# Optimization experiments

Measured on AMD Instinct MI355X. Metric: run time of the kernel, lower is better.

## Reference

```python
import jax, jax.numpy as jnp
import numpy as np


def setup_inputs() -> dict:
    key = jax.random.key(0)
    ks = jax.random.split(key, 7)
    B, IN, OUT, G = 8192, 2048, 2048, 4
    s_i = 1.0 / np.sqrt(IN)
    s_h = 1.0 / np.sqrt(OUT)
    return {
        "x": jax.random.normal(ks[0], (B, IN), jnp.float32),
        "prev_h": jax.random.normal(ks[1], (B, OUT), jnp.float32),
        "prev_c": jax.random.normal(ks[2], (B, OUT), jnp.float32),
        "Wi": jax.random.normal(ks[3], (G, IN, OUT), jnp.float32) * s_i,
        "Wh": jax.random.normal(ks[4], (G, OUT, OUT), jnp.float32) * s_h,
        "bi": jax.random.normal(ks[5], (G, OUT), jnp.float32) * s_i,
        "bh": jax.random.normal(ks[6], (G, OUT), jnp.float32) * s_h,
    }


def reference(x, prev_h, prev_c, Wi, Wh, bi, bh):
    # Two fused GEMMs replacing 8 per-gate Linears (gate order: in, forget, in2, out)
    # gates: [B, 4, OUT]
    gates = (jnp.einsum("bi,gio->bgo", x, Wi) + bi[None]
             + jnp.einsum("bh,gho->bgo", prev_h, Wh) + bh[None])
    in_gate = jax.nn.sigmoid(gates[:, 0])
    forget_gate = jax.nn.sigmoid(gates[:, 1])
    in_gate2 = jax.nn.sigmoid(gates[:, 2])
    out_gate = jax.nn.sigmoid(gates[:, 3])
    next_c = forget_gate * prev_c + in_gate * in_gate2
    # NOTE: faithful to source: out_gate + tanh(next_c) (addition, not multiply)
    next_h = out_gate + jnp.tanh(next_c)
    return next_h, next_c
```

## Files before the change

### kernel.cpp

```cpp
#include <hip/hip_runtime.h>
#include <stdint.h>


#define SZ_ELEMS 16777216
#define HALF_OUT 16777216

typedef __attribute__((ext_vector_type(8))) short bf16x8;
typedef __attribute__((ext_vector_type(4))) float f32x4;
typedef __attribute__((ext_vector_type(8))) unsigned short u16x8;

__device__ __forceinline__ unsigned short f2bf(float f) {
  unsigned int u = __float_as_uint(f);
  u += 0x7FFFu + ((u >> 16) & 1u);
  return (unsigned short)(u >> 16);
}

__device__ __forceinline__ void async16(const void* g, void* l) {
  __builtin_amdgcn_global_load_lds(
      (const __attribute__((address_space(1))) void*)g,
      (__attribute__((address_space(3))) void*)l, 16, 0, 0);
}

__device__ __forceinline__ float sigm(float x) { return 1.f / (1.f + __expf(-x)); }

__global__ void cvt_bf16_kernel(const float* __restrict__ src,
                                unsigned short* __restrict__ dst, int n4) {
  int i = blockIdx.x * blockDim.x + threadIdx.x;
  int stride = gridDim.x * blockDim.x;
  for (; i < n4; i += stride) {
    float4 v = reinterpret_cast<const float4*>(src)[i];
    ushort4 o;
    o.x = f2bf(v.x); o.y = f2bf(v.y); o.z = f2bf(v.z); o.w = f2bf(v.w);
    reinterpret_cast<ushort4*>(dst)[i] = o;
  }
}

__global__ void transpose_w_kernel(const float* __restrict__ Wi, const float* __restrict__ Wh,
                                   unsigned short* __restrict__ Wit, unsigned short* __restrict__ Wht) {
  __shared__ float tile[64][65];
  const int tk = blockIdx.x, to = blockIdx.y, gz = blockIdx.z;
  const float* W = (gz < 4 ? Wi : Wh) + (size_t)(gz & 3) * 4194304;
  unsigned short* Wt = (gz < 4 ? Wit : Wht) + (size_t)(gz & 3) * 4194304;
  const int t = threadIdx.x;
  const int o = t & 63, kr = t >> 6;
#pragma unroll
  for (int p = 0; p < 16; ++p) {
    int k = p * 4 + kr;
    tile[k][o] = W[(size_t)(tk * 64 + k) * 2048 + to * 64 + o];
  }
  __syncthreads();
#pragma unroll
  for (int p = 0; p < 2; ++p) {
    int idx = p * 256 + t;
    int orow = idx >> 3, k0 = (idx & 7) * 8;
    u16x8 v;
#pragma unroll
    for (int i = 0; i < 8; ++i) v[i] = f2bf(tile[k0 + i][orow]);
    *reinterpret_cast<u16x8*>(&Wt[(size_t)(to * 64 + orow) * 2048 + tk * 64 + k0]) = v;
  }
}

#define FENCE asm volatile("" ::: "memory")
#define BARRIER do { FENCE; __builtin_amdgcn_s_barrier(); FENCE; } while (0)
#define VMC6  asm volatile("s_waitcnt vmcnt(6)" ::: "memory")
#define VMC0  asm volatile("s_waitcnt vmcnt(0)" ::: "memory")

__global__ __launch_bounds__(512, 2) void lstm_gemm_kernel(
    const unsigned short* __restrict__ xb, const unsigned short* __restrict__ hb,
    const unsigned short* __restrict__ wit, const unsigned short* __restrict__ wht,
    const float* __restrict__ bi, const float* __restrict__ bh,
    const float* __restrict__ prev_c, float* __restrict__ out) {
  __shared__ char lds[131072];

  const int tid = threadIdx.x;
  const int wave = tid >> 6, lane = tid & 63;
  const int wm = wave >> 2, wn = wave & 3;
  const int bm = blockIdx.x;
  const int bo = blockIdx.y;

  const int kwin = (lane >> 4) << 4;
  const int fswz = (lane & 7) << 4;
  int aro[8], bro[4];
#pragma unroll
  for (int mf = 0; mf < 8; ++mf) aro[mf] = (wm * 128 + mf * 16 + (lane & 15)) * 128;
#pragma unroll
  for (int nf = 0; nf < 4; ++nf) bro[nf] = 32768 + (nf * 64 + wn * 16 + (lane & 15)) * 128;

  const int L0 = tid * 16;
  int agoff[2][2], bgoff[2][2];
#pragma unroll
  for (int h = 0; h < 2; ++h)
#pragma unroll
    for (int j = 0; j < 2; ++j) {
      int L = j * 8192 + L0;
      int row = h * 128 + (L >> 7);
      int c = (L & 127) ^ ((row & 7) << 4);
      agoff[h][j] = row * 4096 + c;
      int g = row >> 6, orow = row & 63;
      bgoff[h][j] = g * 8388608 + orow * 4096 + c;
    }
  const char* pxa = (const char*)xb + (size_t)bm * 1048576;
  const char* pha = (const char*)hb + (size_t)bm * 1048576;
  const char* pwi = (const char*)wit + (size_t)bo * 262144;
  const char* pwh = (const char*)wht + (size_t)bo * 262144;

  auto stageA = [&](int t, int h, int buf) {
    const char* base = (t < 32) ? (pxa + t * 128) : (pha + (t - 32) * 128);
    char* d = lds + buf * 65536 + h * 16384 + L0;
    async16(base + agoff[h][0], d);
    async16(base + agoff[h][1], d + 8192);
  };
  auto stageB = [&](int t, int h, int buf) {
    const char* base = (t < 32) ? (pwi + t * 128) : (pwh + (t - 32) * 128);
    char* d = lds + buf * 65536 + 32768 + h * 16384 + L0;
    async16(base + bgoff[h][0], d);
    async16(base + bgoff[h][1], d + 8192);
  };

  f32x4 acc[8][4];
  const f32x4 zero = {0.f, 0.f, 0.f, 0.f};
#pragma unroll
  for (int mf = 0; mf < 8; ++mf)
#pragma unroll
    for (int nf = 0; nf < 4; ++nf) acc[mf][nf] = zero;

  bf16x8 afrA[4][2];
  bf16x8 afrB[4][2];
  bf16x8 bfr[4][2];

  auto loadAA = [&](int buf) {
    const char* l = lds + buf * 65536;
#pragma unroll
    for (int m = 0; m < 4; ++m)
#pragma unroll
      for (int ks = 0; ks < 2; ++ks)
        afrA[m][ks] = *(const bf16x8*)(l + aro[m] + ((ks * 64 + kwin) ^ fswz));
  };
  auto loadAB = [&](int buf) {
    const char* l = lds + buf * 65536;
#pragma unroll
    for (int m = 0; m < 4; ++m)
#pragma unroll
      for (int ks = 0; ks < 2; ++ks)
        afrB[m][ks] = *(const bf16x8*)(l + aro[4 + m] + ((ks * 64 + kwin) ^ fswz));
  };
  auto loadB0 = [&](int buf) {
    const char* l = lds + buf * 65536;
#pragma unroll
    for (int n = 0; n < 2; ++n)
#pragma unroll
      for (int ks = 0; ks < 2; ++ks)
        bfr[n][ks] = *(const bf16x8*)(l + bro[n] + ((ks * 64 + kwin) ^ fswz));
  };
  auto loadB1 = [&](int buf) {
    const char* l = lds + buf * 65536;
#pragma unroll
    for (int n = 0; n < 2; ++n)
#pragma unroll
      for (int ks = 0; ks < 2; ++ks)
        bfr[2 + n][ks] = *(const bf16x8*)(l + bro[2 + n] + ((ks * 64 + kwin) ^ fswz));
  };
  auto MQ = [&](int mh, int nh) {
    __builtin_amdgcn_s_setprio(1);
#pragma unroll
    for (int ks = 0; ks < 2; ++ks)
#pragma unroll
      for (int n = 0; n < 2; ++n)
#pragma unroll
        for (int m = 0; m < 4; ++m)
          acc[mh * 4 + m][nh * 2 + n] = __builtin_amdgcn_mfma_f32_16x16x32_bf16(
              (mh ? afrB : afrA)[m][ks], bfr[nh * 2 + n][ks],
              acc[mh * 4 + m][nh * 2 + n], 0, 0, 0);
    __builtin_amdgcn_s_setprio(0);
  };

  stageB(0, 0, 0); stageB(0, 1, 0); stageA(0, 0, 0); stageA(0, 1, 0);
  stageB(1, 0, 1); stageB(1, 1, 1); stageA(1, 0, 1);
  VMC6;
  BARRIER;
  loadAA(0); loadB0(0);

  for (int i = 0; i < 31; ++i) {
    const int t1 = 2 * i + 1, t2 = 2 * i + 2, t3 = 2 * i + 3;
    stageA(t1, 1, 1); MQ(0, 0); loadB1(0); BARRIER;
    stageB(t2, 0, 0); MQ(0, 1); loadAB(0); BARRIER;
    stageB(t2, 1, 0); MQ(1, 0); BARRIER;
    stageA(t2, 0, 0); MQ(1, 1); VMC6; loadAA(1); loadB0(1); BARRIER;
    stageA(t2, 1, 0); MQ(0, 0); loadB1(1); BARRIER;
    stageB(t3, 0, 1); MQ(0, 1); loadAB(1); BARRIER;
    stageB(t3, 1, 1); MQ(1, 0); BARRIER;
    stageA(t3, 0, 1); MQ(1, 1); VMC6; loadAA(0); loadB0(0); BARRIER;
  }

  stageA(63, 1, 1); MQ(0, 0); loadB1(0); BARRIER;
  MQ(0, 1); loadAB(0); BARRIER;
  MQ(1, 0); BARRIER;
  MQ(1, 1); VMC0; loadAA(1); loadB0(1); BARRIER;
  MQ(0, 0); loadB1(1); BARRIER;
  MQ(0, 1); loadAB(1); BARRIER;
  MQ(1, 0); BARRIER;
  MQ(1, 1);

  const int col = lane & 15, rg = lane >> 4;
  const int o = bo * 64 + wn * 16 + col;
  float bs[4];
#pragma unroll
  for (int g = 0; g < 4; ++g) bs[g] = bi[g * 2048 + o] + bh[g * 2048 + o];
#pragma unroll
  for (int mf = 0; mf < 8; ++mf) {
    int bbase = bm * 256 + wm * 128 + mf * 16 + rg * 4;
#pragma unroll
    for (int r = 0; r < 4; ++r) {
      int b = bbase + r;
      float gi = sigm(acc[mf][0][r] + bs[0]);
      float gf = sigm(acc[mf][1][r] + bs[1]);
      float g2 = sigm(acc[mf][2][r] + bs[2]);
      float go = sigm(acc[mf][3][r] + bs[3]);
      float c = prev_c[(size_t)b * 2048 + o];
      float nc = gf * c + gi * g2;
      float e = __expf(2.f * nc);
      float nh = go + (e - 1.f) / (e + 1.f);
      out[(size_t)b * 2048 + o] = nh;
      out[(size_t)HALF_OUT + (size_t)b * 2048 + o] = nc;
    }
  }
}

extern "C" void kernel_launch(void* const* d_in, const int* in_sizes, int n_in,
                              void* d_out, int out_size, void* d_ws, size_t ws_size,
                              hipStream_t stream) {
  const float* x  = (const float*)d_in[0];
  const float* ph = (const float*)d_in[1];
  const float* pc = (const float*)d_in[2];
  const float* Wi = (const float*)d_in[3];
  const float* Wh = (const float*)d_in[4];
  const float* bi = (const float*)d_in[5];
  const float* bh = (const float*)d_in[6];
  float* out = (float*)d_out;

  if (ws_size < (size_t)4 * SZ_ELEMS * sizeof(unsigned short)) return;
  unsigned short* xb  = (unsigned short*)d_ws;
  unsigned short* hb  = xb + SZ_ELEMS;
  unsigned short* wit = hb + SZ_ELEMS;
  unsigned short* wht = wit + SZ_ELEMS;

  cvt_bf16_kernel<<<2048, 256, 0, stream>>>(x, xb, 4194304);
  cvt_bf16_kernel<<<2048, 256, 0, stream>>>(ph, hb, 4194304);
  transpose_w_kernel<<<dim3(32, 32, 8), 256, 0, stream>>>(Wi, Wh, wit, wht);
  lstm_gemm_kernel<<<dim3(32, 32), 512, 0, stream>>>(xb, hb, wit, wht, bi, bh, pc, out);
}
```

Measured before the change: 510.7 us.

## Restructure GEMM main loop to cut barriers per K-tile and batch stage loads

Reorganizes the double-buffered pipeline so each half-iteration uses two barriers instead of four. LDS fragment reads are issued before their MFMA quadrants and drained with an explicit lgkmcnt(0) wait, and all four global-to-LDS stage loads for the next tile are grouped. The vmcnt threshold rises from 6 to 8 to match the new count of outstanding loads. The aim is less barrier synchronization and more overlap of global loads with MFMA, with the risk of LDS hazards or more latency exposure if the ordering is wrong.

```diff
diff --git a/kernel.cpp b/kernel.cpp
--- a/kernel.cpp
+++ b/kernel.cpp
@@ -62,7 +62,8 @@
 
 #define FENCE asm volatile("" ::: "memory")
 #define BARRIER do { FENCE; __builtin_amdgcn_s_barrier(); FENCE; } while (0)
-#define VMC6  asm volatile("s_waitcnt vmcnt(6)" ::: "memory")
+#define LGKM0 asm volatile("s_waitcnt lgkmcnt(0)" ::: "memory")
+#define VMC8  asm volatile("s_waitcnt vmcnt(8)" ::: "memory")
 #define VMC0  asm volatile("s_waitcnt vmcnt(0)" ::: "memory")
 
 __global__ __launch_bounds__(512, 2) void lstm_gemm_kernel(
@@ -175,31 +176,32 @@
   };
 
   stageB(0, 0, 0); stageB(0, 1, 0); stageA(0, 0, 0); stageA(0, 1, 0);
-  stageB(1, 0, 1); stageB(1, 1, 1); stageA(1, 0, 1);
-  VMC6;
+  stageB(1, 0, 1); stageB(1, 1, 1); stageA(1, 0, 1); stageA(1, 1, 1);
+  VMC8;
   BARRIER;
   loadAA(0); loadB0(0);
 
   for (int i = 0; i < 31; ++i) {
-    const int t1 = 2 * i + 1, t2 = 2 * i + 2, t3 = 2 * i + 3;
-    stageA(t1, 1, 1); MQ(0, 0); loadB1(0); BARRIER;
-    stageB(t2, 0, 0); MQ(0, 1); loadAB(0); BARRIER;
-    stageB(t2, 1, 0); MQ(1, 0); BARRIER;
-    stageA(t2, 0, 0); MQ(1, 1); VMC6; loadAA(1); loadB0(1); BARRIER;
-    stageA(t2, 1, 0); MQ(0, 0); loadB1(1); BARRIER;
-    stageB(t3, 0, 1); MQ(0, 1); loadAB(1); BARRIER;
-    stageB(t3, 1, 1); MQ(1, 0); BARRIER;
-    stageA(t3, 0, 1); MQ(1, 1); VMC6; loadAA(0); loadB0(0); BARRIER;
-  }
-
-  stageA(63, 1, 1); MQ(0, 0); loadB1(0); BARRIER;
-  MQ(0, 1); loadAB(0); BARRIER;
-  MQ(1, 0); BARRIER;
+    const int t2 = 2 * i + 2, t3 = 2 * i + 3;
+    loadB1(0); MQ(0, 0);
+    loadAB(0); MQ(0, 1); LGKM0; BARRIER;
+    stageB(t2, 0, 0); stageB(t2, 1, 0); MQ(1, 0);
+    stageA(t2, 0, 0); stageA(t2, 1, 0); MQ(1, 1);
+    VMC8; loadAA(1); loadB0(1); BARRIER;
+    loadB1(1); MQ(0, 0);
+    loadAB(1); MQ(0, 1); LGKM0; BARRIER;
+    stageB(t3, 0, 1); stageB(t3, 1, 1); MQ(1, 0);
+    stageA(t3, 0, 1); stageA(t3, 1, 1); MQ(1, 1);
+    VMC8; loadAA(0); loadB0(0); BARRIER;
+  }
+
+  loadB1(0); MQ(0, 0);
+  loadAB(0); MQ(0, 1);
+  MQ(1, 0);
   MQ(1, 1); VMC0; loadAA(1); loadB0(1); BARRIER;
-  MQ(0, 0); loadB1(1); BARRIER;
-  MQ(0, 1); loadAB(1); BARRIER;
-  MQ(1, 0); BARRIER;
-  MQ(1, 1);
+  loadB1(1); MQ(0, 0);
+  loadAB(1); MQ(0, 1);
+  MQ(1, 0); MQ(1, 1);
 
   const int col = lane & 15, rg = lane >> 4;
   const int o = bo * 64 + wn * 16 + col;
```

After: 1.340 ms. +162.4%, slower.
